# Optimization experiments

Hardware: AMD Instinct MI355X
Metric: run time of the kernel (lower is better)

The kernel has to match this reference:

```python
import jax, jax.numpy as jnp
import numpy as np


def gcn_conv(x, edge_index, edge_weight, W, b):
    """Faithful PyG GCNConv: add self-loops (weight 1), symmetric normalization,
    linear transform, weighted sum aggregation at target nodes, then bias."""
    N = x.shape[0]
    loops = jnp.arange(N, dtype=edge_index.dtype)
    row = jnp.concatenate([edge_index[0], loops])  # source j
    col = jnp.concatenate([edge_index[1], loops])  # target i
    ew = jnp.concatenate([edge_weight, jnp.ones((N,), dtype=edge_weight.dtype)])
    deg = jax.ops.segment_sum(ew, col, num_segments=N)  # [N]
    dinv = jnp.where(deg > 0, jax.lax.rsqrt(deg), 0.0)
    norm = dinv[row] * ew * dinv[col]  # [E+N]
    xw = x @ W  # [N, F_out]
    msgs = xw[row] * norm[:, None]  # [E+N, F_out]
    out = jax.ops.segment_sum(msgs, col, num_segments=N)  # [N, F_out]
    return out + b


def setup_inputs() -> dict:
    key = jax.random.key(0)
    k = jax.random.split(key, 8)
    N, E, Fin, Fhid, Fout = 50000, 800000, 128, 128, 64
    x = jax.random.normal(k[0], (N, Fin), dtype=jnp.float32)
    edge_index = jax.random.randint(k[1], (2, E), 0, N, dtype=jnp.int64)
    edge_weight = jax.random.uniform(k[2], (E,), dtype=jnp.float32)
    s0 = 1.0 / np.sqrt(Fin)
    s1 = 1.0 / np.sqrt(Fhid)
    W0 = jax.random.uniform(k[3], (Fin, Fhid), jnp.float32, -s0, s0)
    b0 = jnp.zeros((Fhid,), jnp.float32)
    W1 = jax.random.uniform(k[4], (Fhid, Fout), jnp.float32, -s1, s1)
    b1 = jnp.zeros((Fout,), jnp.float32)
    return {"x": x, "edge_index": edge_index, "edge_weight": edge_weight,
            "W0": W0, "b0": b0, "W1": W1, "b1": b1}


def reference(x, edge_index, edge_weight, W0, b0, W1, b1):
    # Encoder with num_layers=2, drop_p=0.0 (identity), activation=ReLU
    h = gcn_conv(x, edge_index, edge_weight, W0, b0)
    h = jax.nn.relu(h)
    h = gcn_conv(h, edge_index, edge_weight, W1, b1)
    h = jax.nn.relu(h)
    return h
```

## Files before the change

### kernel.cpp

```cpp
#include <hip/hip_runtime.h>

#define MAXDEG 48
#define BSH 6
#define BNODES 64
#define BCAP 2048

typedef unsigned short ushort_t;
typedef __attribute__((ext_vector_type(8))) short short8;
typedef __attribute__((ext_vector_type(4))) float f32x4;

__device__ inline ushort_t f2bf(float f) {
    union { float f; unsigned u; } v;
    v.f = f;
    unsigned r = v.u + 0x7fff + ((v.u >> 16) & 1);
    return (ushort_t)(r >> 16);
}

__device__ inline float bf2f_lo(unsigned u) {
    union { unsigned u; float f; } v;
    v.u = u << 16;
    return v.f;
}

__device__ inline float bf2f_hi(unsigned u) {
    union { unsigned u; float f; } v;
    v.u = u & 0xffff0000u;
    return v.f;
}


__global__ void k_setup(const float* __restrict__ W0, ushort_t* __restrict__ wp0,
                        const float* __restrict__ W1, ushort_t* __restrict__ wp1,
                        int* __restrict__ bcur, int NB) {
    int tid = blockIdx.x * blockDim.x + threadIdx.x;
    int stride = gridDim.x * blockDim.x;
    for (int i = tid; i < NB; i += stride) bcur[i] = 0;
    for (int e = tid; e < 16384; e += stride) {
        int j = e & 7, l = (e >> 3) & 63, ct = e >> 9;
        int t = ct & 7, c = ct >> 3;
        int k = 32 * c + (l >> 4) * 8 + j;
        int n = 16 * t + (l & 15);
        wp0[e] = f2bf(W0[k * 128 + n]);
    }
    for (int e = tid; e < 8192; e += stride) {
        int j = e & 7, l = (e >> 3) & 63, ct = e >> 9;
        int t = ct & 3, c = ct >> 2;
        int k = 32 * c + (l >> 4) * 8 + j;
        int n = 16 * t + (l & 15);
        wp1[e] = f2bf(W1[k * 64 + n]);
    }
}


__global__ __launch_bounds__(256) void k_scatter(const int* __restrict__ row,
                                                 const int* __restrict__ col,
                                                 const float* __restrict__ ew,
                                                 int* __restrict__ bcur,
                                                 uint2* __restrict__ recs, int E, int NB) {
    __shared__ int cnt[1024];
    __shared__ int base[1024];
    const int t = threadIdx.x;
    const size_t e0 = (size_t)blockIdx.x * (256 * 16);
    for (int i = t; i < NB; i += 256) cnt[i] = 0;
    __syncthreads();
    int ck[16], rk[16];
#pragma unroll
    for (int j = 0; j < 16; ++j) {
        size_t e = e0 + (size_t)j * 256 + t;
        ck[j] = -1;
        if (e < (size_t)E) {
            int c = col[e];
            ck[j] = c;
            rk[j] = atomicAdd(&cnt[c >> BSH], 1);
        }
    }
    __syncthreads();
    for (int i = t; i < NB; i += 256) {
        int c = cnt[i];
        base[i] = c ? atomicAdd(&bcur[i], c) : 0;
    }
    __syncthreads();
#pragma unroll
    for (int j = 0; j < 16; ++j) {
        size_t e = e0 + (size_t)j * 256 + t;
        if (e < (size_t)E) {
            int c = ck[j];
            int b = c >> BSH;
            int idx = base[b] + rk[j];
            if (idx < BCAP) {
                uint2 r;
                r.x = (unsigned)row[e] | ((unsigned)(c & (BNODES - 1)) << 16);
                r.y = __float_as_uint(ew[e]);
                recs[(size_t)b * BCAP + idx] = r;
            }
        }
    }
}


__global__ __launch_bounds__(256) void k_ell_build(const uint2* __restrict__ recs,
                                                   const int* __restrict__ bcur,
                                                   uint2* __restrict__ ell,
                                                   int* __restrict__ counts,
                                                   float* __restrict__ dinv, int N) {
    __shared__ uint2 tile[BNODES * MAXDEG];
    __shared__ int cnt[BNODES];
    const int b = blockIdx.x;
    const int t = threadIdx.x;
    if (t < BNODES) cnt[t] = 0;
    __syncthreads();
    const size_t s = (size_t)b * BCAP;
    const int ne = min(bcur[b], BCAP);
    for (int i = t; i < ne; i += 256) {
        uint2 r = recs[s + i];
        int dl = (r.x >> 16) & (BNODES - 1);
        int pos = atomicAdd(&cnt[dl], 1);
        if (pos < MAXDEG) {
            uint2 c;
            c.x = r.x & 0xffffu;
            c.y = r.y;
            tile[dl * MAXDEG + pos] = c;
        }
    }
    __syncthreads();
    const int node0 = b << BSH;
    if (t < BNODES) {
        int node = node0 + t;
        if (node < N) {
            int cn = min(cnt[t], MAXDEG);
            float sum = 1.0f;
            for (int j = 0; j < cn; ++j) sum += __uint_as_float(tile[t * MAXDEG + j].y);
            dinv[node] = rsqrtf(sum);
            counts[node] = cn;
        }
    }
    __syncthreads();
    const int nvalid = min(BNODES, N - node0);
    const int total = nvalid * MAXDEG;
    for (int i = t; i < total; i += 256) {
        int nl = i / MAXDEG;
        int slot = i - nl * MAXDEG;
        if (slot < min(cnt[nl], MAXDEG))
            ell[(size_t)node0 * MAXDEG + i] = tile[i];
    }
}


template <int FO, bool ABF16>
__global__ __launch_bounds__(256) void k_gemm_mfma(const void* __restrict__ Xv,
                                                   const uint4* __restrict__ Wp,
                                                   ushort_t* __restrict__ Y, int N) {
    constexpr int NT = FO >> 4;
    const int wave = threadIdx.x >> 6;
    const int lane = threadIdx.x & 63;
    const int m0 = blockIdx.x * 64 + wave * 16;
    if (m0 >= N) return;
    const int q = lane >> 4;
    const int mr = lane & 15;
    const int rowc = min(m0 + mr, N - 1);

    short8 a[4];
    if (ABF16) {
        const ushort_t* xr = (const ushort_t*)Xv + (size_t)rowc * 128 + q * 8;
#pragma unroll
        for (int c = 0; c < 4; ++c) {
            uint4 v = *(const uint4*)(xr + 32 * c);
            __builtin_memcpy(&a[c], &v, 16);
        }
    } else {
        const float* xr = (const float*)Xv + (size_t)rowc * 128 + q * 8;
#pragma unroll
        for (int c = 0; c < 4; ++c) {
            float4 v0 = *(const float4*)(xr + 32 * c);
            float4 v1 = *(const float4*)(xr + 32 * c + 4);
            a[c][0] = (short)f2bf(v0.x); a[c][1] = (short)f2bf(v0.y);
            a[c][2] = (short)f2bf(v0.z); a[c][3] = (short)f2bf(v0.w);
            a[c][4] = (short)f2bf(v1.x); a[c][5] = (short)f2bf(v1.y);
            a[c][6] = (short)f2bf(v1.z); a[c][7] = (short)f2bf(v1.w);
        }
    }

#pragma unroll
    for (int t = 0; t < NT; ++t) {
        f32x4 acc = {0.0f, 0.0f, 0.0f, 0.0f};
#pragma unroll
        for (int c = 0; c < 4; ++c) {
            uint4 bw = Wp[(size_t)(c * NT + t) * 64 + lane];
            short8 b;
            __builtin_memcpy(&b, &bw, 16);
            acc = __builtin_amdgcn_mfma_f32_16x16x32_bf16(a[c], b, acc, 0, 0, 0);
        }
        const int colbase = 16 * t + mr;
#pragma unroll
        for (int r = 0; r < 4; ++r) {
            int orow = m0 + q * 4 + r;
            if (orow < N) Y[(size_t)orow * FO + colbase] = f2bf(acc[r]);
        }
    }
}


__global__ __launch_bounds__(256) void k_gather128(const int* __restrict__ counts,
                                                   const uint2* __restrict__ ell,
                                                   const float* __restrict__ dinv,
                                                   const unsigned* __restrict__ xwb,
                                                   const float* __restrict__ bias,
                                                   unsigned* __restrict__ h1b, int N) {
    int node = (blockIdx.x * 256 + threadIdx.x) >> 6;
    int lane = threadIdx.x & 63;
    if (node >= N) return;
    float di = dinv[node];
    int cnt = min(counts[node], MAXDEG);

    int sv = 0;
    float wv = 0.0f;
    if (lane < cnt) {
        uint2 rec = ell[(size_t)node * MAXDEG + lane];
        sv = (int)rec.x;
        wv = dinv[sv] * __uint_as_float(rec.y) * di;
    }

    unsigned u0 = xwb[(size_t)node * 64 + lane];
    float2 bb = ((const float2*)bias)[lane];
    float sw = di * di;
    float ax = bb.x + bf2f_lo(u0) * sw;
    float ay = bb.y + bf2f_hi(u0) * sw;

    int j = 0;
    for (; j + 4 <= cnt; j += 4) {
        int s0 = __shfl(sv, j), s1 = __shfl(sv, j + 1), s2 = __shfl(sv, j + 2), s3 = __shfl(sv, j + 3);
        float w0 = __shfl(wv, j), w1 = __shfl(wv, j + 1), w2 = __shfl(wv, j + 2), w3 = __shfl(wv, j + 3);
        unsigned v0 = xwb[(size_t)s0 * 64 + lane];
        unsigned v1 = xwb[(size_t)s1 * 64 + lane];
        unsigned v2 = xwb[(size_t)s2 * 64 + lane];
        unsigned v3 = xwb[(size_t)s3 * 64 + lane];
        ax += bf2f_lo(v0) * w0; ay += bf2f_hi(v0) * w0;
        ax += bf2f_lo(v1) * w1; ay += bf2f_hi(v1) * w1;
        ax += bf2f_lo(v2) * w2; ay += bf2f_hi(v2) * w2;
        ax += bf2f_lo(v3) * w3; ay += bf2f_hi(v3) * w3;
    }
    for (; j < cnt; ++j) {
        int s = __shfl(sv, j);
        float w = __shfl(wv, j);
        unsigned v = xwb[(size_t)s * 64 + lane];
        ax += bf2f_lo(v) * w; ay += bf2f_hi(v) * w;
    }
    unsigned packed = ((unsigned)f2bf(fmaxf(ay, 0.0f)) << 16) | f2bf(fmaxf(ax, 0.0f));
    h1b[(size_t)node * 64 + lane] = packed;
}


__global__ __launch_bounds__(256) void k_gather64_relu(const int* __restrict__ counts,
                                                       const uint2* __restrict__ ell,
                                                       const float* __restrict__ dinv,
                                                       const ushort_t* __restrict__ xwb,
                                                       const float* __restrict__ bias,
                                                       float* __restrict__ h, int N) {
    int node = (blockIdx.x * 256 + threadIdx.x) >> 6;
    int lane = threadIdx.x & 63;
    if (node >= N) return;
    float di = dinv[node];
    int cnt = min(counts[node], MAXDEG);

    int sv = 0;
    float wv = 0.0f;
    if (lane < cnt) {
        uint2 rec = ell[(size_t)node * MAXDEG + lane];
        sv = (int)rec.x;
        wv = dinv[sv] * __uint_as_float(rec.y) * di;
    }

    float acc = bias[lane] + bf2f_lo((unsigned)xwb[(size_t)node * 64 + lane]) * di * di;

    int j = 0;
    for (; j + 4 <= cnt; j += 4) {
        int s0 = __shfl(sv, j), s1 = __shfl(sv, j + 1), s2 = __shfl(sv, j + 2), s3 = __shfl(sv, j + 3);
        float w0 = __shfl(wv, j), w1 = __shfl(wv, j + 1), w2 = __shfl(wv, j + 2), w3 = __shfl(wv, j + 3);
        float v0 = bf2f_lo((unsigned)xwb[(size_t)s0 * 64 + lane]);
        float v1 = bf2f_lo((unsigned)xwb[(size_t)s1 * 64 + lane]);
        float v2 = bf2f_lo((unsigned)xwb[(size_t)s2 * 64 + lane]);
        float v3 = bf2f_lo((unsigned)xwb[(size_t)s3 * 64 + lane]);
        acc += v0 * w0 + v1 * w1 + v2 * w2 + v3 * w3;
    }
    for (; j < cnt; ++j) {
        acc += bf2f_lo((unsigned)xwb[(size_t)__shfl(sv, j) * 64 + lane]) * __shfl(wv, j);
    }
    h[(size_t)node * 64 + lane] = fmaxf(acc, 0.0f);
}


extern "C" void kernel_launch(void* const* d_in, const int* in_sizes, int n_in,
                              void* d_out, int out_size, void* d_ws, size_t ws_size,
                              hipStream_t stream) {
    const float* x  = (const float*)d_in[0];
    const int*   ei = (const int*)d_in[1];
    const float* ew = (const float*)d_in[2];
    const float* W0 = (const float*)d_in[3];
    const float* b0 = (const float*)d_in[4];
    const float* W1 = (const float*)d_in[5];
    const float* b1 = (const float*)d_in[6];
    float* out = (float*)d_out;

    const int Fhid = in_sizes[4];
    const int Fin  = in_sizes[3] / Fhid;
    const int N    = in_sizes[0] / Fin;
    const int E    = in_sizes[2];
    const int NB   = (N + BNODES - 1) >> BSH;

    const int* row = ei;
    const int* col = ei + E;

    char* w = (char*)d_ws;
    auto alloc = [&](size_t bytes) {
        char* p = w;
        w += (bytes + 255) & ~(size_t)255;
        return p;
    };
    float*    dinv   = (float*)alloc((size_t)N * 4);
    int*      counts = (int*)alloc((size_t)N * 4);
    int*      bcur   = (int*)alloc((size_t)NB * 4);
    uint2*    recs   = (uint2*)alloc((size_t)NB * BCAP * 8);
    uint2*    ell    = (uint2*)alloc((size_t)N * MAXDEG * 8);
    ushort_t* xw1b   = (ushort_t*)alloc((size_t)N * 128 * 2);
    unsigned* h1b    = (unsigned*)alloc((size_t)N * 64 * 4);
    ushort_t* xw2b   = (ushort_t*)alloc((size_t)N * 64 * 2);
    ushort_t* wp0    = (ushort_t*)alloc(16384 * 2);
    ushort_t* wp1    = (ushort_t*)alloc(8192 * 2);

    const int T = 256;

    k_setup<<<32, T, 0, stream>>>(W0, wp0, W1, wp1, bcur, NB);
    k_scatter<<<(E + 4095) / 4096, T, 0, stream>>>(row, col, ew, bcur, recs, E, NB);
    k_ell_build<<<NB, T, 0, stream>>>(recs, bcur, ell, counts, dinv, N);

    const int GB = (N + 63) / 64;

    k_gemm_mfma<128, false><<<GB, T, 0, stream>>>(x, (const uint4*)wp0, xw1b, N);
    k_gather128<<<(N + 3) / 4, T, 0, stream>>>(counts, ell, dinv, (const unsigned*)xw1b, b0, h1b, N);

    k_gemm_mfma<64, true><<<GB, T, 0, stream>>>(h1b, (const uint4*)wp1, xw2b, N);
    k_gather64_relu<<<(N + 3) / 4, T, 0, stream>>>(counts, ell, dinv, xw2b, b1, out, N);
}
```

Measured before the change: 191.7 us.

## Fuse scatter with GEMM1 and bucket build with layer-1 gather and GEMM2

Degree is now accumulated with global atomics during the scatter, and the layer-0 GEMM blocks share one launch with the scatter blocks. The ELL build, normalized edge weights, layer-1 aggregation and the layer-2 GEMM are merged into one 512-thread bucket kernel that keeps h1 in shared memory. This removes the h1b round trip and three launches and hoists the normalization out of the final gather. In exchange it adds float atomics on deg (non-deterministic summation order) and more shared memory per block, which may lower occupancy.

```diff
diff --git a/kernel.cpp b/kernel.cpp
--- a/kernel.cpp
+++ b/kernel.cpp
@@ -31,10 +31,11 @@
 
 __global__ void k_setup(const float* __restrict__ W0, ushort_t* __restrict__ wp0,
                         const float* __restrict__ W1, ushort_t* __restrict__ wp1,
-                        int* __restrict__ bcur, int NB) {
+                        int* __restrict__ bcur, float* __restrict__ deg, int NB, int N) {
     int tid = blockIdx.x * blockDim.x + threadIdx.x;
     int stride = gridDim.x * blockDim.x;
     for (int i = tid; i < NB; i += stride) bcur[i] = 0;
+    for (int i = tid; i < N; i += stride) deg[i] = 0.0f;
     for (int e = tid; e < 16384; e += stride) {
         int j = e & 7, l = (e >> 3) & 63, ct = e >> 9;
         int t = ct & 7, c = ct >> 3;
@@ -52,26 +53,90 @@
 }
 
 
-__global__ __launch_bounds__(256) void k_scatter(const int* __restrict__ row,
-                                                 const int* __restrict__ col,
-                                                 const float* __restrict__ ew,
-                                                 int* __restrict__ bcur,
-                                                 uint2* __restrict__ recs, int E, int NB) {
+template <int FO, bool ABF16>
+__device__ inline void gemm_body(const void* __restrict__ Xv,
+                                 const uint4* __restrict__ Wp,
+                                 ushort_t* __restrict__ Y, int N, int bid) {
+    constexpr int NT = FO >> 4;
+    const int wave = threadIdx.x >> 6;
+    const int lane = threadIdx.x & 63;
+    const int m0 = bid * 64 + wave * 16;
+    if (m0 >= N) return;
+    const int q = lane >> 4;
+    const int mr = lane & 15;
+    const int rowc = min(m0 + mr, N - 1);
+
+    short8 a[4];
+    if (ABF16) {
+        const ushort_t* xr = (const ushort_t*)Xv + (size_t)rowc * 128 + q * 8;
+#pragma unroll
+        for (int c = 0; c < 4; ++c) {
+            uint4 v = *(const uint4*)(xr + 32 * c);
+            __builtin_memcpy(&a[c], &v, 16);
+        }
+    } else {
+        const float* xr = (const float*)Xv + (size_t)rowc * 128 + q * 8;
+#pragma unroll
+        for (int c = 0; c < 4; ++c) {
+            float4 v0 = *(const float4*)(xr + 32 * c);
+            float4 v1 = *(const float4*)(xr + 32 * c + 4);
+            a[c][0] = (short)f2bf(v0.x); a[c][1] = (short)f2bf(v0.y);
+            a[c][2] = (short)f2bf(v0.z); a[c][3] = (short)f2bf(v0.w);
+            a[c][4] = (short)f2bf(v1.x); a[c][5] = (short)f2bf(v1.y);
+            a[c][6] = (short)f2bf(v1.z); a[c][7] = (short)f2bf(v1.w);
+        }
+    }
+
+#pragma unroll
+    for (int t = 0; t < NT; ++t) {
+        f32x4 acc = {0.0f, 0.0f, 0.0f, 0.0f};
+#pragma unroll
+        for (int c = 0; c < 4; ++c) {
+            uint4 bw = Wp[(size_t)(c * NT + t) * 64 + lane];
+            short8 b;
+            __builtin_memcpy(&b, &bw, 16);
+            acc = __builtin_amdgcn_mfma_f32_16x16x32_bf16(a[c], b, acc, 0, 0, 0);
+        }
+        const int colbase = 16 * t + mr;
+#pragma unroll
+        for (int r = 0; r < 4; ++r) {
+            int orow = m0 + q * 4 + r;
+            if (orow < N) Y[(size_t)orow * FO + colbase] = f2bf(acc[r]);
+        }
+    }
+}
+
+
+__global__ __launch_bounds__(256) void k_scatter_gemm1(
+        const int* __restrict__ row, const int* __restrict__ col,
+        const float* __restrict__ ew, int* __restrict__ bcur,
+        uint2* __restrict__ recs, float* __restrict__ deg, int E, int NB,
+        const float* __restrict__ x, const uint4* __restrict__ wp0,
+        ushort_t* __restrict__ xw1b, int N, int GB) {
     __shared__ int cnt[1024];
     __shared__ int base[1024];
+    if ((int)blockIdx.x < GB) {
+        gemm_body<128, false>(x, wp0, xw1b, N, blockIdx.x);
+        return;
+    }
+    const int bid = blockIdx.x - GB;
     const int t = threadIdx.x;
-    const size_t e0 = (size_t)blockIdx.x * (256 * 16);
+    const size_t e0 = (size_t)bid * (256 * 16);
     for (int i = t; i < NB; i += 256) cnt[i] = 0;
     __syncthreads();
     int ck[16], rk[16];
+    float wk[16];
 #pragma unroll
     for (int j = 0; j < 16; ++j) {
         size_t e = e0 + (size_t)j * 256 + t;
         ck[j] = -1;
         if (e < (size_t)E) {
             int c = col[e];
+            float w = ew[e];
             ck[j] = c;
+            wk[j] = w;
             rk[j] = atomicAdd(&cnt[c >> BSH], 1);
+            atomicAdd(&deg[c], w);
         }
     }
     __syncthreads();
@@ -82,15 +147,15 @@
     __syncthreads();
 #pragma unroll
     for (int j = 0; j < 16; ++j) {
-        size_t e = e0 + (size_t)j * 256 + t;
-        if (e < (size_t)E) {
+        if (ck[j] >= 0) {
+            size_t e = e0 + (size_t)j * 256 + t;
             int c = ck[j];
             int b = c >> BSH;
             int idx = base[b] + rk[j];
             if (idx < BCAP) {
                 uint2 r;
                 r.x = (unsigned)row[e] | ((unsigned)(c & (BNODES - 1)) << 16);
-                r.y = __float_as_uint(ew[e]);
+                r.y = __float_as_uint(wk[j]);
                 recs[(size_t)b * BCAP + idx] = r;
             }
         }
@@ -98,21 +163,25 @@
 }
 
 
-__global__ __launch_bounds__(256) void k_ell_build(const uint2* __restrict__ recs,
-                                                   const int* __restrict__ bcur,
-                                                   uint2* __restrict__ ell,
-                                                   int* __restrict__ counts,
-                                                   float* __restrict__ dinv, int N) {
+__global__ __launch_bounds__(512) void k_bucket(
+        const uint2* __restrict__ recs, const int* __restrict__ bcur,
+        const float* __restrict__ deg, const unsigned* __restrict__ xw1b,
+        const uint4* __restrict__ wp1, const float* __restrict__ b0,
+        uint2* __restrict__ ell, int* __restrict__ counts,
+        ushort_t* __restrict__ xw2b, int N) {
     __shared__ uint2 tile[BNODES * MAXDEG];
     __shared__ int cnt[BNODES];
+    __shared__ ushort_t h1[BNODES][136];
     const int b = blockIdx.x;
     const int t = threadIdx.x;
+    const int node0 = b << BSH;
     if (t < BNODES) cnt[t] = 0;
     __syncthreads();
-    const size_t s = (size_t)b * BCAP;
+
+    const size_t s0 = (size_t)b * BCAP;
     const int ne = min(bcur[b], BCAP);
-    for (int i = t; i < ne; i += 256) {
-        uint2 r = recs[s + i];
+    for (int i = t; i < ne; i += 512) {
+        uint2 r = recs[s0 + i];
         int dl = (r.x >> 16) & (BNODES - 1);
         int pos = atomicAdd(&cnt[dl], 1);
         if (pos < MAXDEG) {
@@ -123,93 +192,98 @@
         }
     }
     __syncthreads();
-    const int node0 = b << BSH;
-    if (t < BNODES) {
-        int node = node0 + t;
-        if (node < N) {
-            int cn = min(cnt[t], MAXDEG);
-            float sum = 1.0f;
-            for (int j = 0; j < cn; ++j) sum += __uint_as_float(tile[t * MAXDEG + j].y);
-            dinv[node] = rsqrtf(sum);
-            counts[node] = cn;
-        }
-    }
-    __syncthreads();
-    const int nvalid = min(BNODES, N - node0);
-    const int total = nvalid * MAXDEG;
-    for (int i = t; i < total; i += 256) {
-        int nl = i / MAXDEG;
-        int slot = i - nl * MAXDEG;
-        if (slot < min(cnt[nl], MAXDEG))
-            ell[(size_t)node0 * MAXDEG + i] = tile[i];
-    }
-}
-
-
-template <int FO, bool ABF16>
-__global__ __launch_bounds__(256) void k_gemm_mfma(const void* __restrict__ Xv,
-                                                   const uint4* __restrict__ Wp,
-                                                   ushort_t* __restrict__ Y, int N) {
-    constexpr int NT = FO >> 4;
-    const int wave = threadIdx.x >> 6;
-    const int lane = threadIdx.x & 63;
-    const int m0 = blockIdx.x * 64 + wave * 16;
-    if (m0 >= N) return;
-    const int q = lane >> 4;
-    const int mr = lane & 15;
-    const int rowc = min(m0 + mr, N - 1);
-
-    short8 a[4];
-    if (ABF16) {
-        const ushort_t* xr = (const ushort_t*)Xv + (size_t)rowc * 128 + q * 8;
+
+    for (int i = t; i < BNODES * MAXDEG; i += 512) {
+        int nl = i / MAXDEG, sl = i - nl * MAXDEG;
+        int node = node0 + nl;
+        if (node >= N) continue;
+        int cc = min(cnt[nl], MAXDEG);
+        if (sl == 0) counts[node] = cc;
+        if (sl < cc) {
+            uint2 c = tile[i];
+            int s = (int)c.x;
+            float w = rsqrtf(deg[s] + 1.0f) * __uint_as_float(c.y) *
+                      rsqrtf(deg[node] + 1.0f);
+            c.y = __float_as_uint(w);
+            tile[i] = c;
+            ell[(size_t)node * MAXDEG + sl] = c;
+        }
+    }
+    __syncthreads();
+
+    const int wave = t >> 6, lane = t & 63;
+    for (int k = 0; k < 8; ++k) {
+        int nl = wave * 8 + k;
+        int node = node0 + nl;
+        if (node >= N) continue;
+        int cc = min(cnt[nl], MAXDEG);
+        float di = rsqrtf(deg[node] + 1.0f);
+        unsigned u0 = xw1b[(size_t)node * 64 + lane];
+        float2 bb = ((const float2*)b0)[lane];
+        float sw = di * di;
+        float ax = bb.x + bf2f_lo(u0) * sw;
+        float ay = bb.y + bf2f_hi(u0) * sw;
+        const uint2* tr = &tile[nl * MAXDEG];
+        int j = 0;
+        for (; j + 4 <= cc; j += 4) {
+            uint2 t0 = tr[j], t1 = tr[j + 1], t2 = tr[j + 2], t3 = tr[j + 3];
+            unsigned v0 = xw1b[(size_t)t0.x * 64 + lane];
+            unsigned v1 = xw1b[(size_t)t1.x * 64 + lane];
+            unsigned v2 = xw1b[(size_t)t2.x * 64 + lane];
+            unsigned v3 = xw1b[(size_t)t3.x * 64 + lane];
+            float w0 = __uint_as_float(t0.y), w1 = __uint_as_float(t1.y);
+            float w2 = __uint_as_float(t2.y), w3 = __uint_as_float(t3.y);
+            ax += bf2f_lo(v0) * w0; ay += bf2f_hi(v0) * w0;
+            ax += bf2f_lo(v1) * w1; ay += bf2f_hi(v1) * w1;
+            ax += bf2f_lo(v2) * w2; ay += bf2f_hi(v2) * w2;
+            ax += bf2f_lo(v3) * w3; ay += bf2f_hi(v3) * w3;
+        }
+        for (; j < cc; ++j) {
+            uint2 tj = tr[j];
+            unsigned v = xw1b[(size_t)tj.x * 64 + lane];
+            float w = __uint_as_float(tj.y);
+            ax += bf2f_lo(v) * w; ay += bf2f_hi(v) * w;
+        }
+        unsigned packed = ((unsigned)f2bf(fmaxf(ay, 0.0f)) << 16) | f2bf(fmaxf(ax, 0.0f));
+        *(unsigned*)&h1[nl][2 * lane] = packed;
+    }
+    __syncthreads();
+
+    const int q = lane >> 4, mr = lane & 15;
+    for (int p = wave; p < 16; p += 8) {
+        const int strip = p & 3, tt = p >> 2;
+        const int arow = strip * 16 + mr;
+        short8 a[4];
+#pragma unroll
+        for (int c = 0; c < 4; ++c)
+            __builtin_memcpy(&a[c], &h1[arow][32 * c + 8 * q], 16);
+        f32x4 acc = {0.0f, 0.0f, 0.0f, 0.0f};
 #pragma unroll
         for (int c = 0; c < 4; ++c) {
-            uint4 v = *(const uint4*)(xr + 32 * c);
-            __builtin_memcpy(&a[c], &v, 16);
-        }
-    } else {
-        const float* xr = (const float*)Xv + (size_t)rowc * 128 + q * 8;
-#pragma unroll
-        for (int c = 0; c < 4; ++c) {
-            float4 v0 = *(const float4*)(xr + 32 * c);
-            float4 v1 = *(const float4*)(xr + 32 * c + 4);
-            a[c][0] = (short)f2bf(v0.x); a[c][1] = (short)f2bf(v0.y);
-            a[c][2] = (short)f2bf(v0.z); a[c][3] = (short)f2bf(v0.w);
-            a[c][4] = (short)f2bf(v1.x); a[c][5] = (short)f2bf(v1.y);
-            a[c][6] = (short)f2bf(v1.z); a[c][7] = (short)f2bf(v1.w);
-        }
-    }
-
-#pragma unroll
-    for (int t = 0; t < NT; ++t) {
-        f32x4 acc = {0.0f, 0.0f, 0.0f, 0.0f};
-#pragma unroll
-        for (int c = 0; c < 4; ++c) {
-            uint4 bw = Wp[(size_t)(c * NT + t) * 64 + lane];
-            short8 b;
-            __builtin_memcpy(&b, &bw, 16);
-            acc = __builtin_amdgcn_mfma_f32_16x16x32_bf16(a[c], b, acc, 0, 0, 0);
-        }
-        const int colbase = 16 * t + mr;
+            uint4 bw = wp1[(size_t)(c * 4 + tt) * 64 + lane];
+            short8 bf;
+            __builtin_memcpy(&bf, &bw, 16);
+            acc = __builtin_amdgcn_mfma_f32_16x16x32_bf16(a[c], bf, acc, 0, 0, 0);
+        }
+        const int colb = 16 * tt + mr;
 #pragma unroll
         for (int r = 0; r < 4; ++r) {
-            int orow = m0 + q * 4 + r;
-            if (orow < N) Y[(size_t)orow * FO + colbase] = f2bf(acc[r]);
-        }
-    }
-}
-
-
-__global__ __launch_bounds__(256) void k_gather128(const int* __restrict__ counts,
-                                                   const uint2* __restrict__ ell,
-                                                   const float* __restrict__ dinv,
-                                                   const unsigned* __restrict__ xwb,
-                                                   const float* __restrict__ bias,
-                                                   unsigned* __restrict__ h1b, int N) {
+            int orow = node0 + strip * 16 + q * 4 + r;
+            if (orow < N) xw2b[(size_t)orow * 64 + colb] = f2bf(acc[r]);
+        }
+    }
+}
+
+
+__global__ __launch_bounds__(256) void k_gather64(const int* __restrict__ counts,
+                                                  const uint2* __restrict__ ell,
+                                                  const float* __restrict__ deg,
+                                                  const ushort_t* __restrict__ xwb,
+                                                  const float* __restrict__ bias,
+                                                  float* __restrict__ h, int N) {
     int node = (blockIdx.x * 256 + threadIdx.x) >> 6;
     int lane = threadIdx.x & 63;
     if (node >= N) return;
-    float di = dinv[node];
     int cnt = min(counts[node], MAXDEG);
 
     int sv = 0;
@@ -217,59 +291,10 @@
     if (lane < cnt) {
         uint2 rec = ell[(size_t)node * MAXDEG + lane];
         sv = (int)rec.x;
-        wv = dinv[sv] * __uint_as_float(rec.y) * di;
-    }
-
-    unsigned u0 = xwb[(size_t)node * 64 + lane];
-    float2 bb = ((const float2*)bias)[lane];
-    float sw = di * di;
-    float ax = bb.x + bf2f_lo(u0) * sw;
-    float ay = bb.y + bf2f_hi(u0) * sw;
-
-    int j = 0;
-    for (; j + 4 <= cnt; j += 4) {
-        int s0 = __shfl(sv, j), s1 = __shfl(sv, j + 1), s2 = __shfl(sv, j + 2), s3 = __shfl(sv, j + 3);
-        float w0 = __shfl(wv, j), w1 = __shfl(wv, j + 1), w2 = __shfl(wv, j + 2), w3 = __shfl(wv, j + 3);
-        unsigned v0 = xwb[(size_t)s0 * 64 + lane];
-        unsigned v1 = xwb[(size_t)s1 * 64 + lane];
-        unsigned v2 = xwb[(size_t)s2 * 64 + lane];
-        unsigned v3 = xwb[(size_t)s3 * 64 + lane];
-        ax += bf2f_lo(v0) * w0; ay += bf2f_hi(v0) * w0;
-        ax += bf2f_lo(v1) * w1; ay += bf2f_hi(v1) * w1;
-        ax += bf2f_lo(v2) * w2; ay += bf2f_hi(v2) * w2;
-        ax += bf2f_lo(v3) * w3; ay += bf2f_hi(v3) * w3;
-    }
-    for (; j < cnt; ++j) {
-        int s = __shfl(sv, j);
-        float w = __shfl(wv, j);
-        unsigned v = xwb[(size_t)s * 64 + lane];
-        ax += bf2f_lo(v) * w; ay += bf2f_hi(v) * w;
-    }
-    unsigned packed = ((unsigned)f2bf(fmaxf(ay, 0.0f)) << 16) | f2bf(fmaxf(ax, 0.0f));
-    h1b[(size_t)node * 64 + lane] = packed;
-}
-
-
-__global__ __launch_bounds__(256) void k_gather64_relu(const int* __restrict__ counts,
-                                                       const uint2* __restrict__ ell,
-                                                       const float* __restrict__ dinv,
-                                                       const ushort_t* __restrict__ xwb,
-                                                       const float* __restrict__ bias,
-                                                       float* __restrict__ h, int N) {
-    int node = (blockIdx.x * 256 + threadIdx.x) >> 6;
-    int lane = threadIdx.x & 63;
-    if (node >= N) return;
-    float di = dinv[node];
-    int cnt = min(counts[node], MAXDEG);
-
-    int sv = 0;
-    float wv = 0.0f;
-    if (lane < cnt) {
-        uint2 rec = ell[(size_t)node * MAXDEG + lane];
-        sv = (int)rec.x;
-        wv = dinv[sv] * __uint_as_float(rec.y) * di;
-    }
-
+        wv = __uint_as_float(rec.y);
+    }
+
+    float di = rsqrtf(deg[node] + 1.0f);
     float acc = bias[lane] + bf2f_lo((unsigned)xwb[(size_t)node * 64 + lane]) * di * di;
 
     int j = 0;
@@ -316,28 +341,23 @@
         w += (bytes + 255) & ~(size_t)255;
         return p;
     };
-    float*    dinv   = (float*)alloc((size_t)N * 4);
+    float*    deg    = (float*)alloc((size_t)N * 4);
     int*      counts = (int*)alloc((size_t)N * 4);
     int*      bcur   = (int*)alloc((size_t)NB * 4);
     uint2*    recs   = (uint2*)alloc((size_t)NB * BCAP * 8);
     uint2*    ell    = (uint2*)alloc((size_t)N * MAXDEG * 8);
     ushort_t* xw1b   = (ushort_t*)alloc((size_t)N * 128 * 2);
-    unsigned* h1b    = (unsigned*)alloc((size_t)N * 64 * 4);
     ushort_t* xw2b   = (ushort_t*)alloc((size_t)N * 64 * 2);
     ushort_t* wp0    = (ushort_t*)alloc(16384 * 2);
     ushort_t* wp1    = (ushort_t*)alloc(8192 * 2);
 
-    const int T = 256;
-
-    k_setup<<<32, T, 0, stream>>>(W0, wp0, W1, wp1, bcur, NB);
-    k_scatter<<<(E + 4095) / 4096, T, 0, stream>>>(row, col, ew, bcur, recs, E, NB);
-    k_ell_build<<<NB, T, 0, stream>>>(recs, bcur, ell, counts, dinv, N);
-
     const int GB = (N + 63) / 64;
-
-    k_gemm_mfma<128, false><<<GB, T, 0, stream>>>(x, (const uint4*)wp0, xw1b, N);
-    k_gather128<<<(N + 3) / 4, T, 0, stream>>>(counts, ell, dinv, (const unsigned*)xw1b, b0, h1b, N);
-
-    k_gemm_mfma<64, true><<<GB, T, 0, stream>>>(h1b, (const uint4*)wp1, xw2b, N);
-    k_gather64_relu<<<(N + 3) / 4, T, 0, stream>>>(counts, ell, dinv, xw2b, b1, out, N);
-}
+    const int SB = (E + 4095) / 4096;
+
+    k_setup<<<64, 256, 0, stream>>>(W0, wp0, W1, wp1, bcur, deg, NB, N);
+    k_scatter_gemm1<<<GB + SB, 256, 0, stream>>>(row, col, ew, bcur, recs, deg, E, NB,
+                                                 x, (const uint4*)wp0, xw1b, N, GB);
+    k_bucket<<<NB, 512, 0, stream>>>(recs, bcur, deg, (const unsigned*)xw1b,
+                                     (const uint4*)wp1, b0, ell, counts, xw2b, N);
+    k_gather64<<<(N + 3) / 4, 256, 0, stream>>>(counts, ell, deg, xw2b, b1, out, N);
+}
```

After: 220.8 us. 15.2% more time.

## Fuse layer-1 gather with layer-2 GEMM via shared-memory tile; shrink scatter blocks

Applied to the files above, without the earlier changes.

The layer-1 aggregation kernel now writes each 16-node tile of bf16 hidden activations into shared memory and immediately runs the 128x64 MFMA for layer 2. This drops the h1 intermediate buffer and one kernel launch, along with its global write and read. Separately, the edge scatter kernel processes 1024 edges per block instead of 4096, giving more blocks and fewer registers per thread at the cost of more global atomics on the bucket cursors. The fused kernel has each wave handle four nodes serially, followed by a block barrier.

```diff
diff --git a/kernel.cpp b/kernel.cpp
--- a/kernel.cpp
+++ b/kernel.cpp
@@ -60,12 +60,12 @@
     __shared__ int cnt[1024];
     __shared__ int base[1024];
     const int t = threadIdx.x;
-    const size_t e0 = (size_t)blockIdx.x * (256 * 16);
+    const size_t e0 = (size_t)blockIdx.x * 1024;
     for (int i = t; i < NB; i += 256) cnt[i] = 0;
     __syncthreads();
-    int ck[16], rk[16];
-#pragma unroll
-    for (int j = 0; j < 16; ++j) {
+    int ck[4], rk[4];
+#pragma unroll
+    for (int j = 0; j < 4; ++j) {
         size_t e = e0 + (size_t)j * 256 + t;
         ck[j] = -1;
         if (e < (size_t)E) {
@@ -81,9 +81,9 @@
     }
     __syncthreads();
 #pragma unroll
-    for (int j = 0; j < 16; ++j) {
-        size_t e = e0 + (size_t)j * 256 + t;
-        if (e < (size_t)E) {
+    for (int j = 0; j < 4; ++j) {
+        if (ck[j] >= 0) {
+            size_t e = e0 + (size_t)j * 256 + t;
             int c = ck[j];
             int b = c >> BSH;
             int idx = base[b] + rk[j];
@@ -146,11 +146,9 @@
 }
 
 
-template <int FO, bool ABF16>
-__global__ __launch_bounds__(256) void k_gemm_mfma(const void* __restrict__ Xv,
-                                                   const uint4* __restrict__ Wp,
-                                                   ushort_t* __restrict__ Y, int N) {
-    constexpr int NT = FO >> 4;
+__global__ __launch_bounds__(256) void k_gemm1(const float* __restrict__ X,
+                                               const uint4* __restrict__ Wp,
+                                               ushort_t* __restrict__ Y, int N) {
     const int wave = threadIdx.x >> 6;
     const int lane = threadIdx.x & 63;
     const int m0 = blockIdx.x * 64 + wave * 16;
@@ -160,32 +158,23 @@
     const int rowc = min(m0 + mr, N - 1);
 
     short8 a[4];
-    if (ABF16) {
-        const ushort_t* xr = (const ushort_t*)Xv + (size_t)rowc * 128 + q * 8;
+    const float* xr = X + (size_t)rowc * 128 + q * 8;
+#pragma unroll
+    for (int c = 0; c < 4; ++c) {
+        float4 v0 = *(const float4*)(xr + 32 * c);
+        float4 v1 = *(const float4*)(xr + 32 * c + 4);
+        a[c][0] = (short)f2bf(v0.x); a[c][1] = (short)f2bf(v0.y);
+        a[c][2] = (short)f2bf(v0.z); a[c][3] = (short)f2bf(v0.w);
+        a[c][4] = (short)f2bf(v1.x); a[c][5] = (short)f2bf(v1.y);
+        a[c][6] = (short)f2bf(v1.z); a[c][7] = (short)f2bf(v1.w);
+    }
+
+#pragma unroll
+    for (int t = 0; t < 8; ++t) {
+        f32x4 acc = {0.0f, 0.0f, 0.0f, 0.0f};
 #pragma unroll
         for (int c = 0; c < 4; ++c) {
-            uint4 v = *(const uint4*)(xr + 32 * c);
-            __builtin_memcpy(&a[c], &v, 16);
-        }
-    } else {
-        const float* xr = (const float*)Xv + (size_t)rowc * 128 + q * 8;
-#pragma unroll
-        for (int c = 0; c < 4; ++c) {
-            float4 v0 = *(const float4*)(xr + 32 * c);
-            float4 v1 = *(const float4*)(xr + 32 * c + 4);
-            a[c][0] = (short)f2bf(v0.x); a[c][1] = (short)f2bf(v0.y);
-            a[c][2] = (short)f2bf(v0.z); a[c][3] = (short)f2bf(v0.w);
-            a[c][4] = (short)f2bf(v1.x); a[c][5] = (short)f2bf(v1.y);
-            a[c][6] = (short)f2bf(v1.z); a[c][7] = (short)f2bf(v1.w);
-        }
-    }
-
-#pragma unroll
-    for (int t = 0; t < NT; ++t) {
-        f32x4 acc = {0.0f, 0.0f, 0.0f, 0.0f};
-#pragma unroll
-        for (int c = 0; c < 4; ++c) {
-            uint4 bw = Wp[(size_t)(c * NT + t) * 64 + lane];
+            uint4 bw = Wp[(size_t)(c * 8 + t) * 64 + lane];
             short8 b;
             __builtin_memcpy(&b, &bw, 16);
             acc = __builtin_amdgcn_mfma_f32_16x16x32_bf16(a[c], b, acc, 0, 0, 0);
@@ -194,59 +183,87 @@
 #pragma unroll
         for (int r = 0; r < 4; ++r) {
             int orow = m0 + q * 4 + r;
-            if (orow < N) Y[(size_t)orow * FO + colbase] = f2bf(acc[r]);
-        }
-    }
-}
-
-
-__global__ __launch_bounds__(256) void k_gather128(const int* __restrict__ counts,
-                                                   const uint2* __restrict__ ell,
-                                                   const float* __restrict__ dinv,
-                                                   const unsigned* __restrict__ xwb,
-                                                   const float* __restrict__ bias,
-                                                   unsigned* __restrict__ h1b, int N) {
-    int node = (blockIdx.x * 256 + threadIdx.x) >> 6;
-    int lane = threadIdx.x & 63;
-    if (node >= N) return;
-    float di = dinv[node];
-    int cnt = min(counts[node], MAXDEG);
-
-    int sv = 0;
-    float wv = 0.0f;
-    if (lane < cnt) {
-        uint2 rec = ell[(size_t)node * MAXDEG + lane];
-        sv = (int)rec.x;
-        wv = dinv[sv] * __uint_as_float(rec.y) * di;
-    }
-
-    unsigned u0 = xwb[(size_t)node * 64 + lane];
-    float2 bb = ((const float2*)bias)[lane];
-    float sw = di * di;
-    float ax = bb.x + bf2f_lo(u0) * sw;
-    float ay = bb.y + bf2f_hi(u0) * sw;
-
-    int j = 0;
-    for (; j + 4 <= cnt; j += 4) {
-        int s0 = __shfl(sv, j), s1 = __shfl(sv, j + 1), s2 = __shfl(sv, j + 2), s3 = __shfl(sv, j + 3);
-        float w0 = __shfl(wv, j), w1 = __shfl(wv, j + 1), w2 = __shfl(wv, j + 2), w3 = __shfl(wv, j + 3);
-        unsigned v0 = xwb[(size_t)s0 * 64 + lane];
-        unsigned v1 = xwb[(size_t)s1 * 64 + lane];
-        unsigned v2 = xwb[(size_t)s2 * 64 + lane];
-        unsigned v3 = xwb[(size_t)s3 * 64 + lane];
-        ax += bf2f_lo(v0) * w0; ay += bf2f_hi(v0) * w0;
-        ax += bf2f_lo(v1) * w1; ay += bf2f_hi(v1) * w1;
-        ax += bf2f_lo(v2) * w2; ay += bf2f_hi(v2) * w2;
-        ax += bf2f_lo(v3) * w3; ay += bf2f_hi(v3) * w3;
-    }
-    for (; j < cnt; ++j) {
-        int s = __shfl(sv, j);
-        float w = __shfl(wv, j);
-        unsigned v = xwb[(size_t)s * 64 + lane];
-        ax += bf2f_lo(v) * w; ay += bf2f_hi(v) * w;
-    }
-    unsigned packed = ((unsigned)f2bf(fmaxf(ay, 0.0f)) << 16) | f2bf(fmaxf(ax, 0.0f));
-    h1b[(size_t)node * 64 + lane] = packed;
+            if (orow < N) Y[(size_t)orow * 128 + colbase] = f2bf(acc[r]);
+        }
+    }
+}
+
+
+__global__ __launch_bounds__(256) void k_gather128_gemm2(
+        const int* __restrict__ counts, const uint2* __restrict__ ell,
+        const float* __restrict__ dinv, const unsigned* __restrict__ xwb,
+        const float* __restrict__ b0, const uint4* __restrict__ wp1,
+        ushort_t* __restrict__ xw2b, int N) {
+    __shared__ ushort_t h1[16][136];
+    const int wave = threadIdx.x >> 6, lane = threadIdx.x & 63;
+    const int node0 = blockIdx.x * 16;
+
+#pragma unroll
+    for (int k = 0; k < 4; ++k) {
+        const int nl = wave * 4 + k;
+        const int node = node0 + nl;
+        unsigned packed = 0u;
+        if (node < N) {
+            float di = dinv[node];
+            int cnt = min(counts[node], MAXDEG);
+            int sv = 0;
+            float wv = 0.0f;
+            if (lane < cnt) {
+                uint2 rec = ell[(size_t)node * MAXDEG + lane];
+                sv = (int)rec.x;
+                wv = dinv[sv] * __uint_as_float(rec.y) * di;
+            }
+            unsigned u0 = xwb[(size_t)node * 64 + lane];
+            float2 bb = ((const float2*)b0)[lane];
+            float sw = di * di;
+            float ax = bb.x + bf2f_lo(u0) * sw;
+            float ay = bb.y + bf2f_hi(u0) * sw;
+            int j = 0;
+            for (; j + 4 <= cnt; j += 4) {
+                int s0 = __shfl(sv, j), s1 = __shfl(sv, j + 1),
+                    s2 = __shfl(sv, j + 2), s3 = __shfl(sv, j + 3);
+                float w0 = __shfl(wv, j), w1 = __shfl(wv, j + 1),
+                      w2 = __shfl(wv, j + 2), w3 = __shfl(wv, j + 3);
+                unsigned v0 = xwb[(size_t)s0 * 64 + lane];
+                unsigned v1 = xwb[(size_t)s1 * 64 + lane];
+                unsigned v2 = xwb[(size_t)s2 * 64 + lane];
+                unsigned v3 = xwb[(size_t)s3 * 64 + lane];
+                ax += bf2f_lo(v0) * w0; ay += bf2f_hi(v0) * w0;
+                ax += bf2f_lo(v1) * w1; ay += bf2f_hi(v1) * w1;
+                ax += bf2f_lo(v2) * w2; ay += bf2f_hi(v2) * w2;
+                ax += bf2f_lo(v3) * w3; ay += bf2f_hi(v3) * w3;
+            }
+            for (; j < cnt; ++j) {
+                int s = __shfl(sv, j);
+                float w = __shfl(wv, j);
+                unsigned v = xwb[(size_t)s * 64 + lane];
+                ax += bf2f_lo(v) * w; ay += bf2f_hi(v) * w;
+            }
+            packed = ((unsigned)f2bf(fmaxf(ay, 0.0f)) << 16) | f2bf(fmaxf(ax, 0.0f));
+        }
+        *(unsigned*)&h1[nl][2 * lane] = packed;
+    }
+    __syncthreads();
+
+    const int q = lane >> 4, mr = lane & 15;
+    short8 a[4];
+#pragma unroll
+    for (int c = 0; c < 4; ++c)
+        __builtin_memcpy(&a[c], &h1[mr][32 * c + 8 * q], 16);
+    f32x4 acc = {0.0f, 0.0f, 0.0f, 0.0f};
+#pragma unroll
+    for (int c = 0; c < 4; ++c) {
+        uint4 bw = wp1[(size_t)(c * 4 + wave) * 64 + lane];
+        short8 bf;
+        __builtin_memcpy(&bf, &bw, 16);
+        acc = __builtin_amdgcn_mfma_f32_16x16x32_bf16(a[c], bf, acc, 0, 0, 0);
+    }
+    const int colb = 16 * wave + mr;
+#pragma unroll
+    for (int r = 0; r < 4; ++r) {
+        int orow = node0 + q * 4 + r;
+        if (orow < N) xw2b[(size_t)orow * 64 + colb] = f2bf(acc[r]);
+    }
 }
 
 
@@ -322,22 +339,19 @@
     uint2*    recs   = (uint2*)alloc((size_t)NB * BCAP * 8);
     uint2*    ell    = (uint2*)alloc((size_t)N * MAXDEG * 8);
     ushort_t* xw1b   = (ushort_t*)alloc((size_t)N * 128 * 2);
-    unsigned* h1b    = (unsigned*)alloc((size_t)N * 64 * 4);
     ushort_t* xw2b   = (ushort_t*)alloc((size_t)N * 64 * 2);
     ushort_t* wp0    = (ushort_t*)alloc(16384 * 2);
     ushort_t* wp1    = (ushort_t*)alloc(8192 * 2);
 
     const int T = 256;
+    const int GB = (N + 63) / 64;
 
     k_setup<<<32, T, 0, stream>>>(W0, wp0, W1, wp1, bcur, NB);
-    k_scatter<<<(E + 4095) / 4096, T, 0, stream>>>(row, col, ew, bcur, recs, E, NB);
+    k_scatter<<<(E + 1023) / 1024, T, 0, stream>>>(row, col, ew, bcur, recs, E, NB);
     k_ell_build<<<NB, T, 0, stream>>>(recs, bcur, ell, counts, dinv, N);
-
-    const int GB = (N + 63) / 64;
-
-    k_gemm_mfma<128, false><<<GB, T, 0, stream>>>(x, (const uint4*)wp0, xw1b, N);
-    k_gather128<<<(N + 3) / 4, T, 0, stream>>>(counts, ell, dinv, (const unsigned*)xw1b, b0, h1b, N);
-
-    k_gemm_mfma<64, true><<<GB, T, 0, stream>>>(h1b, (const uint4*)wp1, xw2b, N);
+    k_gemm1<<<GB, T, 0, stream>>>(x, (const uint4*)wp0, xw1b, N);
+    k_gather128_gemm2<<<(N + 15) / 16, T, 0, stream>>>(counts, ell, dinv,
+                                                       (const unsigned*)xw1b, b0,
+                                                       (const uint4*)wp1, xw2b, N);
     k_gather64_relu<<<(N + 3) / 4, T, 0, stream>>>(counts, ell, dinv, xw2b, b1, out, N);
 }
```

Measured after the change: 200.6 us. 4.6% more time.
